# Performance work log

Hardware: AMD Instinct MI355X
Metric: run time of the kernel (lower is better)

Reference implementation:

```python
import jax, jax.numpy as jnp
import numpy as np

DIM = 256
D_STATE = 16
D_CONV = 4
EXPAND = 2
D_INNER = DIM * EXPAND          # 512
DT_RANK = DIM // 16             # 16


def _dwconv(x_bcl, w, b, pad):
    # depthwise 1d conv; x_bcl: (B, C, L), w: (C, 1, K)
    out = jax.lax.conv_general_dilated(
        x_bcl, w, window_strides=(1,), padding=[pad],
        feature_group_count=x_bcl.shape[1],
        dimension_numbers=('NCH', 'OIH', 'NCH'))
    return out + b[None, :, None]


def _forward(x, ln_w, ln_b, W_in, conv_w, conv_b, W_xproj, W_dt, b_dt,
             A_log, D_ssm, W_outp, c1_w, c1_b, c2_w, c2_b, c3_w, c3_b,
             W_out, b_out, W_skip, b_skip):
    Bsz, C = x.shape[:2]
    img_dims = x.shape[2:]
    L = int(np.prod(img_dims))
    xf = x.reshape(Bsz, C, L).transpose(0, 2, 1)          # (B, L, C)
    # LayerNorm over channel dim
    mu = jnp.mean(xf, axis=-1, keepdims=True)
    var = jnp.var(xf, axis=-1, keepdims=True)
    xn = (xf - mu) / jnp.sqrt(var + 1e-5) * ln_w + ln_b   # (B, L, C)

    # ---------------- Mamba block ----------------
    xz = xn @ W_in.T                                      # (B, L, 2*Di)
    xi, z = jnp.split(xz, 2, axis=-1)
    k = conv_w.shape[-1]
    # causal depthwise conv (pad left d_conv-1, truncate to L), then silu
    xc = _dwconv(xi.transpose(0, 2, 1), conv_w, conv_b, (k - 1, 0))
    xc = jax.nn.silu(xc).transpose(0, 2, 1)               # (B, L, Di)
    x_dbl = xc @ W_xproj.T                                # (B, L, dt_rank + 2*N)
    dt = x_dbl[..., :DT_RANK]
    B_s = x_dbl[..., DT_RANK:DT_RANK + D_STATE]           # (B, L, N)
    C_s = x_dbl[..., DT_RANK + D_STATE:]                  # (B, L, N)
    delta = jax.nn.softplus(dt @ W_dt.T + b_dt)           # (B, L, Di)
    A = -jnp.exp(A_log)                                   # (Di, N)
    dA = jnp.exp(delta[..., None] * A)                    # (B, L, Di, N)
    dBu = (delta * xc)[..., None] * B_s[:, :, None, :]    # (B, L, Di, N)

    def step(h, inp):
        dA_t, dBu_t, c_t = inp
        h = dA_t * h + dBu_t                              # (B, Di, N)
        y = jnp.einsum('bdn,bn->bd', h, c_t)
        return h, y

    h0 = jnp.zeros((Bsz, D_INNER, D_STATE), dtype=x.dtype)
    _, ys = jax.lax.scan(
        step, h0,
        (dA.transpose(1, 0, 2, 3), dBu.transpose(1, 0, 2, 3), C_s.transpose(1, 0, 2)))
    y = ys.transpose(1, 0, 2) + D_ssm * xc                # (B, L, Di)
    y = y * jax.nn.silu(z)
    x_ssm = y @ W_outp.T                                  # (B, L, C)

    # ---------------- multi-scale depthwise convs ----------------
    xnT = xn.transpose(0, 2, 1)                           # (B, C, L)

    def msconv(w, b):
        kk = w.shape[-1]
        return jax.nn.silu(_dwconv(xnT, w, b, (kk // 2, kk // 2))).transpose(0, 2, 1)

    combined = x_ssm + msconv(c1_w, c1_b) + msconv(c2_w, c2_b) + msconv(c3_w, c3_b)
    out = combined @ W_out.T + b_out + xn @ W_skip.T + b_skip
    out = out.transpose(0, 2, 1).reshape(x.shape)
    return out + x


def setup_inputs() -> dict:
    key = jax.random.key(0)
    ks = jax.random.split(key, 12)

    def rn(k, shape, s=0.02):
        return jax.random.normal(k, shape, dtype=jnp.float32) * s

    return {
        'x': jax.random.normal(ks[0], (2, DIM, 64, 64), dtype=jnp.float32),
        'ln_w': jnp.ones((DIM,), jnp.float32),
        'ln_b': jnp.zeros((DIM,), jnp.float32),
        'W_in': rn(ks[1], (2 * D_INNER, DIM)),
        'conv_w': rn(ks[2], (D_INNER, 1, D_CONV), 0.1),
        'conv_b': jnp.zeros((D_INNER,), jnp.float32),
        'W_xproj': rn(ks[3], (DT_RANK + 2 * D_STATE, D_INNER)),
        'W_dt': rn(ks[4], (D_INNER, DT_RANK), 0.1),
        'b_dt': jnp.full((D_INNER,), -4.0, jnp.float32),  # softplus(-4) ~ 0.018, stable dt
        'A_log': jnp.log(jnp.broadcast_to(
            jnp.arange(1, D_STATE + 1, dtype=jnp.float32), (D_INNER, D_STATE))),
        'D_ssm': jnp.ones((D_INNER,), jnp.float32),
        'W_outp': rn(ks[5], (DIM, D_INNER)),
        'c1_w': rn(ks[6], (DIM, 1, 3), 0.1),
        'c1_b': jnp.zeros((DIM,), jnp.float32),
        'c2_w': rn(ks[7], (DIM, 1, 5), 0.1),
        'c2_b': jnp.zeros((DIM,), jnp.float32),
        'c3_w': rn(ks[8], (DIM, 1, 7), 0.1),
        'c3_b': jnp.zeros((DIM,), jnp.float32),
        'W_out': rn(ks[9], (DIM, DIM)),
        'b_out': jnp.zeros((DIM,), jnp.float32),
        'W_skip': rn(ks[10], (DIM, DIM)),
        'b_skip': jnp.zeros((DIM,), jnp.float32),
    }


def reference(x, ln_w, ln_b, W_in, conv_w, conv_b, W_xproj, W_dt, b_dt,
              A_log, D_ssm, W_outp, c1_w, c1_b, c2_w, c2_b, c3_w, c3_b,
              W_out, b_out, W_skip, b_skip):
    return _forward(x, ln_w, ln_b, W_in, conv_w, conv_b, W_xproj, W_dt, b_dt,
                    A_log, D_ssm, W_outp, c1_w, c1_b, c2_w, c2_b, c3_w, c3_b,
                    W_out, b_out, W_skip, b_skip)
```

## Files before the change

### kernel.cpp

```cpp
#include <hip/hip_runtime.h>
#include <hip/hip_bf16.h>
#include <math.h>
#include <cstddef>

#define BSZ 2
#define DM 256
#define LSEQ 4096
#define DIN 512
#define DXZ 1024
#define DS 16
#define RANK 16
#define GXP 48
#define LC 32
#define NC 128
#define CSTRIDE (BSZ * DIN * 16)

typedef __attribute__((ext_vector_type(8))) short short8;
typedef __attribute__((ext_vector_type(4))) float f32x4;
struct bf4 { __hip_bfloat16 v[4]; };

__device__ __forceinline__ float silu_f(float x){ return x / (1.f + __expf(-x)); }
__device__ __forceinline__ float softplus_f(float x){ return fmaxf(x, 0.f) + log1pf(__expf(-fabsf(x))); }
__device__ __forceinline__ float b2f(__hip_bfloat16 v){ return __bfloat162float(v); }
__device__ __forceinline__ __hip_bfloat16 f2b(float v){ return __float2bfloat16(v); }

__device__ __forceinline__ void gl_lds16(const void* g, void* s){
    __builtin_amdgcn_global_load_lds((const __attribute__((address_space(1))) void*)g,
                                     (__attribute__((address_space(3))) void*)s, 16, 0, 0);
}

__global__ __launch_bounds__(256) void k_ln(const float* __restrict__ x,
                                            const float* __restrict__ lnw,
                                            const float* __restrict__ lnb,
                                            __hip_bfloat16* __restrict__ xnb){
    __shared__ float tile[DM * 33];
    __shared__ float rsum[8][32], rsq[8][32];
    __shared__ float mu_s[32], rs_s[32];
    int b  = blockIdx.x >> 7;
    int l0 = (blockIdx.x & 127) << 5;
    int tid = threadIdx.x;
    const float* xb = x + (size_t)b * DM * LSEQ;
    int lls = tid & 31, chi = tid >> 5;
    for (int cc = 0; cc < 32; ++cc){
        int c = cc * 8 + chi;
        tile[c * 33 + lls] = xb[(size_t)c * LSEQ + l0 + lls];
    }
    __syncthreads();
    int part = tid >> 5, l = tid & 31;
    float s = 0.f, sq = 0.f;
    for (int i = 0; i < 32; ++i){
        float v = tile[(part * 32 + i) * 33 + l];
        s += v; sq += v * v;
    }
    rsum[part][l] = s; rsq[part][l] = sq;
    __syncthreads();
    if (tid < 32){
        float ts = 0.f, tq = 0.f;
        for (int p = 0; p < 8; ++p){ ts += rsum[p][tid]; tq += rsq[p][tid]; }
        float mu  = ts * (1.f / DM);
        float var = tq * (1.f / DM) - mu * mu;
        mu_s[tid] = mu;
        rs_s[tid] = rsqrtf(var + 1e-5f);
    }
    __syncthreads();
    int c0 = tid & 63, lh = tid >> 6;
    for (int i = 0; i < 8; ++i){
        int ll = lh + 4 * i;
        float mu = mu_s[ll], rs = rs_s[ll];
        __hip_bfloat16* orow = xnb + (size_t)(b * LSEQ + l0 + ll) * 512;
        for (int j = 0; j < 4; ++j){
            int c = c0 + 64 * j;
            orow[c] = f2b((tile[c * 33 + ll] - mu) * rs * lnw[c] + lnb[c]);
        }
    }
}

__global__ __launch_bounds__(256) void k_cvtw(const float* __restrict__ W_in, const float* __restrict__ W_xproj,
                                              const float* __restrict__ W_outp, const float* __restrict__ W_out,
                                              const float* __restrict__ W_skip, const float* __restrict__ b_out,
                                              const float* __restrict__ b_skip,
                                              __hip_bfloat16* __restrict__ Winb, __hip_bfloat16* __restrict__ Wxpb,
                                              __hip_bfloat16* __restrict__ Wopb, __hip_bfloat16* __restrict__ Wcb,
                                              float* __restrict__ bc){
    int i0 = blockIdx.x * 256 + threadIdx.x;
    const int T = 256 * 256;
    for (int j = i0; j < 1024 * 256; j += T) Winb[j] = f2b(W_in[j]);
    for (int j = i0; j < 64 * 512; j += T){
        int r = j >> 9;
        Wxpb[j] = f2b(r < GXP ? W_xproj[r * 512 + (j & 511)] : 0.f);
    }
    for (int j = i0; j < 256 * 512; j += T) Wopb[j] = f2b(W_outp[j]);
    for (int j = i0; j < 256 * 512; j += T){
        int n = j >> 9, k = j & 511;
        Wcb[j] = f2b(k < 256 ? W_out[n * 256 + k] : W_skip[n * 256 + (k - 256)]);
    }
    if (i0 < 256) bc[i0] = b_out[i0] + b_skip[i0];
}

template<int EPI, int BM = 128, int BN = 64>
__global__ __launch_bounds__(256) void k_mgemm(const __hip_bfloat16* __restrict__ A, int lda,
                                               const __hip_bfloat16* __restrict__ W,
                                               const float* __restrict__ bias,
                                               void* __restrict__ Cv, int ldc,
                                               int N, int K,
                                               const float* __restrict__ xres = nullptr){
    constexpr int SA  = BM / 8;
    constexpr int SAW = SA / 4;
    constexpr int SB  = BN / 8;
    constexpr int SBW = SB / 4;
    constexpr int WROWS = BM / 2;
    constexpr int WCOLS = BN / 2;
    constexpr int MI = WROWS / 16;
    constexpr int NI = WCOLS / 16;
    __shared__ __align__(16) __hip_bfloat16 As[BM * 64];
    __shared__ __align__(16) __hip_bfloat16 Ws[BN * 64];
    __shared__ float tileT[(EPI & 16) ? 64 * 65 : 1];
    const int tid = threadIdx.x;
    const int wave = tid >> 6, lane = tid & 63;
    const int brow = blockIdx.x * BM, bcol = blockIdx.y * BN;
    const int wm = wave >> 1, wn = wave & 1;

    const int a_row = lane >> 3;
    const int a_chk = lane & 7;
    const int a_scol = ((a_chk ^ a_row) * 8);

    const int lrow = lane & 15;
    const int kc = lane >> 4;
    const int r7 = lrow & 7;

    f32x4 acc[MI][NI] = {};

    for (int k0 = 0; k0 < K; k0 += 64){
#pragma unroll
        for (int j = 0; j < SAW; ++j){
            int seg = wave * SAW + j;
            const __hip_bfloat16* src = A + (size_t)(brow + seg * 8 + a_row) * lda + k0 + a_scol;
            gl_lds16(src, &As[seg * 512]);
        }
#pragma unroll
        for (int j = 0; j < SBW; ++j){
            int seg = wave * SBW + j;
            const __hip_bfloat16* src = W + (size_t)(bcol + seg * 8 + a_row) * K + k0 + a_scol;
            gl_lds16(src, &Ws[seg * 512]);
        }
        __syncthreads();
#pragma unroll
        for (int kk = 0; kk < 2; ++kk){
            int kchunk = kk * 4 + kc;
            short8 af[MI], bfr[NI];
#pragma unroll
            for (int mi = 0; mi < MI; ++mi){
                int row = wm * WROWS + mi * 16 + lrow;
                af[mi] = *(const short8*)&As[row * 64 + ((kchunk ^ r7) * 8)];
            }
#pragma unroll
            for (int ni = 0; ni < NI; ++ni){
                int row = wn * WCOLS + ni * 16 + lrow;
                bfr[ni] = *(const short8*)&Ws[row * 64 + ((kchunk ^ r7) * 8)];
            }
#pragma unroll
            for (int mi = 0; mi < MI; ++mi)
#pragma unroll
                for (int ni = 0; ni < NI; ++ni)
                    acc[mi][ni] = __builtin_amdgcn_mfma_f32_16x16x32_bf16(af[mi], bfr[ni], acc[mi][ni], 0, 0, 0);
        }
        __syncthreads();
    }

    if (EPI & 16){
#pragma unroll
        for (int ni = 0; ni < NI; ++ni){
            int nl = wn * WCOLS + ni * 16 + lrow;
#pragma unroll
            for (int mi = 0; mi < MI; ++mi){
                int ml = wm * WROWS + mi * 16 + kc * 4;
#pragma unroll
                for (int r = 0; r < 4; ++r)
                    tileT[nl * 65 + ml + r] = acc[mi][ni][r];
            }
        }
        __syncthreads();
        int b = brow >> 12, l0 = brow & 4095;
        int lr = tid & 63, nr = tid >> 6;
        float* out = (float*)Cv;
#pragma unroll
        for (int rr = 0; rr < 16; ++rr){
            int n = rr * 4 + nr;
            size_t o = (size_t)(b * DM + bcol + n) * LSEQ + l0 + lr;
            out[o] = tileT[n * 65 + lr] + bias[bcol + n] + xres[o];
        }
        return;
    }

#pragma unroll
    for (int ni = 0; ni < NI; ++ni){
        int n = bcol + wn * WCOLS + ni * 16 + lrow;
        if (n >= N) continue;
        float bv = (EPI & 1) ? bias[n] : 0.f;
#pragma unroll
        for (int mi = 0; mi < MI; ++mi){
            int m0 = brow + wm * WROWS + mi * 16 + kc * 4;
#pragma unroll
            for (int r = 0; r < 4; ++r){
                float v = acc[mi][ni][r] + bv;
                if (EPI & 8) ((__hip_bfloat16*)Cv)[(size_t)(m0 + r) * ldc + n] = f2b(v);
                else         ((float*)Cv)[(size_t)(m0 + r) * ldc + n] = v;
            }
        }
    }
}

__global__ __launch_bounds__(256) void k_dtgemm(const float* __restrict__ A, int lda,
                                                const float* __restrict__ Wt,
                                                const float* __restrict__ bias,
                                                __hip_bfloat16* __restrict__ C, int ldc){
    __shared__ float As[16][68];
    __shared__ float Ws[16][68];
    int bm = blockIdx.x * 64, bn = blockIdx.y * 64;
    int tid = threadIdx.x;
    int a_m = tid >> 2, a_k = (tid & 3) * 4;
    int tx = tid & 15, ty = tid >> 4;
    float acc[4][4] = {};
    {
        float4 av = *(const float4*)(A + (size_t)(bm + a_m) * lda + a_k);
        As[a_k + 0][a_m] = av.x; As[a_k + 1][a_m] = av.y;
        As[a_k + 2][a_m] = av.z; As[a_k + 3][a_m] = av.w;
        float4 wv = *(const float4*)(Wt + (size_t)(bn + a_m) * 16 + a_k);
        Ws[a_k + 0][a_m] = wv.x; Ws[a_k + 1][a_m] = wv.y;
        Ws[a_k + 2][a_m] = wv.z; Ws[a_k + 3][a_m] = wv.w;
        __syncthreads();
#pragma unroll
        for (int k = 0; k < 16; ++k){
            float4 a4 = *(const float4*)&As[k][ty * 4];
            float4 b4 = *(const float4*)&Ws[k][tx * 4];
            acc[0][0] += a4.x * b4.x; acc[0][1] += a4.x * b4.y; acc[0][2] += a4.x * b4.z; acc[0][3] += a4.x * b4.w;
            acc[1][0] += a4.y * b4.x; acc[1][1] += a4.y * b4.y; acc[1][2] += a4.y * b4.z; acc[1][3] += a4.y * b4.w;
            acc[2][0] += a4.z * b4.x; acc[2][1] += a4.z * b4.y; acc[2][2] += a4.z * b4.z; acc[2][3] += a4.z * b4.w;
            acc[3][0] += a4.w * b4.x; acc[3][1] += a4.w * b4.y; acc[3][2] += a4.w * b4.z; acc[3][3] += a4.w * b4.w;
        }
    }
    int n = bn + tx * 4;
    float4 bb = *(const float4*)(bias + n);
#pragma unroll
    for (int i = 0; i < 4; ++i){
        int m = bm + ty * 4 + i;
        __hip_bfloat16* cp = C + (size_t)m * ldc + n;
        cp[0] = f2b(softplus_f(acc[i][0] + bb.x));
        cp[1] = f2b(softplus_f(acc[i][1] + bb.y));
        cp[2] = f2b(softplus_f(acc[i][2] + bb.z));
        cp[3] = f2b(softplus_f(acc[i][3] + bb.w));
    }
}

__global__ __launch_bounds__(256) void k_conv(const __hip_bfloat16* __restrict__ xz,
                                              const float* __restrict__ cw,
                                              const float* __restrict__ cb,
                                              __hip_bfloat16* __restrict__ xc){
    int idx = blockIdx.x * 256 + threadIdx.x;
    int d4 = (idx & 127) * 4;
    int bl = idx >> 7;
    int l  = bl & (LSEQ - 1);
    const __hip_bfloat16* base = xz + (size_t)bl * DXZ + d4;
    float4 bias = *(const float4*)(cb + d4);
    float acc[4] = {bias.x, bias.y, bias.z, bias.w};
    float4 w0 = *(const float4*)(cw + (d4 + 0) * 4);
    float4 w1 = *(const float4*)(cw + (d4 + 1) * 4);
    float4 w2 = *(const float4*)(cw + (d4 + 2) * 4);
    float4 w3 = *(const float4*)(cw + (d4 + 3) * 4);
    const float* wj[4] = {(const float*)&w0, (const float*)&w1, (const float*)&w2, (const float*)&w3};
#pragma unroll
    for (int t = 0; t < 4; ++t){
        int ls = l - (3 - t);
        if (ls >= 0){
            bf4 v = *(const bf4*)(base - (size_t)(3 - t) * DXZ);
#pragma unroll
            for (int j = 0; j < 4; ++j) acc[j] += wj[j][t] * b2f(v.v[j]);
        }
    }
    bf4 o;
#pragma unroll
    for (int j = 0; j < 4; ++j) o.v[j] = f2b(silu_f(acc[j]));
    *(bf4*)(xc + (size_t)bl * DIN + d4) = o;
}

__global__ __launch_bounds__(512) void k_scan1(const __hip_bfloat16* __restrict__ delta,
                                               const __hip_bfloat16* __restrict__ xc,
                                               const float* __restrict__ xdbl,
                                               const float* __restrict__ A_log,
                                               float* __restrict__ Acar,
                                               float* __restrict__ Bcar){
    int bx = blockIdx.x;
    int dh = bx & 1;
    int c  = (bx >> 1) & (NC - 1);
    int b  = bx >> 8;
    int tid = threadIdx.x;
    int dloc = tid >> 1, nh = tid & 1;
    int d = dh * 256 + dloc;
    int n0 = nh * 8;
    __shared__ float Bs[LC][DS];
    {
        int t = tid >> 4, n = tid & 15;
        Bs[t][n] = xdbl[(size_t)(b * LSEQ + c * LC + t) * GXP + RANK + n];
    }
    __syncthreads();
    float Av[8];
    float a1 = -__expf(A_log[d * 16]);
    bool fast = true;
#pragma unroll
    for (int j = 0; j < 8; ++j){
        Av[j] = -__expf(A_log[d * 16 + n0 + j]);
        fast = fast && (fabsf(Av[j] - (float)(n0 + j + 1) * a1) <= 1e-4f * fabsf(Av[j]) + 1e-7f);
    }
    float ap[8], ac[8];
#pragma unroll
    for (int j = 0; j < 8; ++j){ ap[j] = 1.f; ac[j] = 0.f; }
    const __hip_bfloat16* dp = delta + (size_t)(b * LSEQ + c * LC) * DIN + d;
    const __hip_bfloat16* xp = xc    + (size_t)(b * LSEQ + c * LC) * DIN + d;
    if (fast){
        for (int t = 0; t < LC; ++t){
            float de = b2f(dp[(size_t)t * DIN]);
            float u  = de * b2f(xp[(size_t)t * DIN]);
            float p  = __expf(de * a1);
            float p2 = p * p, p4 = p2 * p2, p8 = p4 * p4;
            float da = nh ? p8 * p : p;
#pragma unroll
            for (int j = 0; j < 8; ++j){
                ap[j] *= da;
                ac[j] = da * ac[j] + u * Bs[t][n0 + j];
                da *= p;
            }
        }
    } else {
        for (int t = 0; t < LC; ++t){
            float de = b2f(dp[(size_t)t * DIN]);
            float u  = de * b2f(xp[(size_t)t * DIN]);
#pragma unroll
            for (int j = 0; j < 8; ++j){
                float da = __expf(de * Av[j]);
                ap[j] *= da;
                ac[j] = da * ac[j] + u * Bs[t][n0 + j];
            }
        }
    }
    size_t o = (size_t)c * CSTRIDE + (size_t)(b * DIN + d) * 16 + n0;
    *(float4*)(Acar + o)     = make_float4(ap[0], ap[1], ap[2], ap[3]);
    *(float4*)(Acar + o + 4) = make_float4(ap[4], ap[5], ap[6], ap[7]);
    *(float4*)(Bcar + o)     = make_float4(ac[0], ac[1], ac[2], ac[3]);
    *(float4*)(Bcar + o + 4) = make_float4(ac[4], ac[5], ac[6], ac[7]);
}

__global__ __launch_bounds__(256) void k_scan2(const float* __restrict__ Acar,
                                               const float* __restrict__ Bcar,
                                               float* __restrict__ hinit){
    __shared__ float a_s[NC][33];
    __shared__ float b_s[NC][33];
    __shared__ float h_s[NC][33];
    const int tid = threadIdx.x;
    const int idx0 = blockIdx.x * 32;
    const int s_ld = tid & 31, cr = tid >> 5;
#pragma unroll
    for (int r = 0; r < 16; ++r){
        int c = r * 8 + cr;
        size_t g = (size_t)c * CSTRIDE + idx0 + s_ld;
        a_s[c][s_ld] = Acar[g];
        b_s[c][s_ld] = Bcar[g];
    }
    __syncthreads();
    const int lane = tid & 63, w = tid >> 6;
#pragma unroll
    for (int i = 0; i < 8; ++i){
        int s = w * 8 + i;
        float a0 = a_s[2 * lane][s],     b0 = b_s[2 * lane][s];
        float a1 = a_s[2 * lane + 1][s], b1 = b_s[2 * lane + 1][s];
        float av = a0 * a1, bv = a1 * b0 + b1;
#pragma unroll
        for (int d2 = 1; d2 < 64; d2 <<= 1){
            float ao = __shfl_up(av, d2);
            float bo = __shfl_up(bv, d2);
            if (lane >= d2){ bv = av * bo + bv; av = ao * av; }
        }
        float ax = __shfl_up(av, 1), bx = __shfl_up(bv, 1);
        if (lane == 0){ ax = 1.f; bx = 0.f; }
        h_s[2 * lane][s]     = bx;
        h_s[2 * lane + 1][s] = a0 * bx + b0;
    }
    __syncthreads();
#pragma unroll
    for (int r = 0; r < 16; ++r){
        int c = r * 8 + cr;
        hinit[(size_t)c * CSTRIDE + idx0 + s_ld] = h_s[c][s_ld];
    }
}

__global__ __launch_bounds__(512) void k_scan3(const __hip_bfloat16* __restrict__ delta,
                                               const __hip_bfloat16* __restrict__ xc,
                                               const __hip_bfloat16* __restrict__ xz,
                                               const float* __restrict__ xdbl,
                                               const float* __restrict__ A_log,
                                               const float* __restrict__ D_ssm,
                                               const float* __restrict__ hinit,
                                               __hip_bfloat16* __restrict__ y){
    int bx = blockIdx.x;
    int dh = bx & 1;
    int c  = (bx >> 1) & (NC - 1);
    int b  = bx >> 8;
    int tid = threadIdx.x;
    int dloc = tid >> 1, nh = tid & 1;
    int d = dh * 256 + dloc;
    int n0 = nh * 8;
    __shared__ float Bs[LC][DS], Cs[LC][DS];
    {
        int t = tid >> 4, n = tid & 15;
        size_t r = (size_t)(b * LSEQ + c * LC + t) * GXP;
        Bs[t][n] = xdbl[r + RANK + n];
        Cs[t][n] = xdbl[r + RANK + DS + n];
    }
    __syncthreads();
    float Av[8];
    float a1 = -__expf(A_log[d * 16]);
    bool fast = true;
#pragma unroll
    for (int j = 0; j < 8; ++j){
        Av[j] = -__expf(A_log[d * 16 + n0 + j]);
        fast = fast && (fabsf(Av[j] - (float)(n0 + j + 1) * a1) <= 1e-4f * fabsf(Av[j]) + 1e-7f);
    }
    float h[8];
    size_t ho = (size_t)c * CSTRIDE + (size_t)(b * DIN + d) * 16 + n0;
    {
        float4 h0 = *(const float4*)(hinit + ho);
        float4 h1 = *(const float4*)(hinit + ho + 4);
        h[0] = h0.x; h[1] = h0.y; h[2] = h0.z; h[3] = h0.w;
        h[4] = h1.x; h[5] = h1.y; h[6] = h1.z; h[7] = h1.w;
    }
    float Dd = D_ssm[d];
    size_t rb = (size_t)(b * LSEQ + c * LC);
    if (fast){
        for (int t = 0; t < LC; ++t){
            size_t row = rb + t;
            float de  = b2f(delta[row * DIN + d]);
            float xcv = b2f(xc[row * DIN + d]);
            float u = de * xcv;
            float p  = __expf(de * a1);
            float p2 = p * p, p4 = p2 * p2, p8 = p4 * p4;
            float da = nh ? p8 * p : p;
            float yv = 0.f;
#pragma unroll
            for (int j = 0; j < 8; ++j){
                h[j] = da * h[j] + u * Bs[t][n0 + j];
                yv += h[j] * Cs[t][n0 + j];
                da *= p;
            }
            yv += __shfl_xor(yv, 1);
            if (nh == 0){
                float zv = b2f(xz[row * DXZ + DIN + d]);
                y[row * DIN + d] = f2b((yv + Dd * xcv) * silu_f(zv));
            }
        }
    } else {
        for (int t = 0; t < LC; ++t){
            size_t row = rb + t;
            float de  = b2f(delta[row * DIN + d]);
            float xcv = b2f(xc[row * DIN + d]);
            float u = de * xcv;
            float yv = 0.f;
#pragma unroll
            for (int j = 0; j < 8; ++j){
                float da = __expf(de * Av[j]);
                h[j] = da * h[j] + u * Bs[t][n0 + j];
                yv += h[j] * Cs[t][n0 + j];
            }
            yv += __shfl_xor(yv, 1);
            if (nh == 0){
                float zv = b2f(xz[row * DXZ + DIN + d]);
                y[row * DIN + d] = f2b((yv + Dd * xcv) * silu_f(zv));
            }
        }
    }
}

__global__ __launch_bounds__(256) void k_msconv(const __hip_bfloat16* __restrict__ xnb,
                                                const __hip_bfloat16* __restrict__ xssm,
                                                const float* __restrict__ c1w, const float* __restrict__ c1b,
                                                const float* __restrict__ c2w, const float* __restrict__ c2b,
                                                const float* __restrict__ c3w, const float* __restrict__ c3b,
                                                __hip_bfloat16* __restrict__ Acomb){
    int idx = blockIdx.x * 256 + threadIdx.x;
    int cch = idx & (DM - 1);
    int bl  = idx >> 8;
    int l   = bl & (LSEQ - 1);
    int bL  = bl - l;
    float a1 = c1b[cch], a2 = c2b[cch], a3 = c3b[cch];
#pragma unroll
    for (int j = -3; j <= 3; ++j){
        int ll = l + j;
        if ((unsigned)ll < LSEQ){
            float v = b2f(xnb[(size_t)(bL + ll) * 512 + cch]);
            if (j >= -1 && j <= 1) a1 += c1w[cch * 3 + (j + 1)] * v;
            if (j >= -2 && j <= 2) a2 += c2w[cch * 5 + (j + 2)] * v;
            a3 += c3w[cch * 7 + (j + 3)] * v;
        }
    }
    float res = b2f(xssm[(size_t)bl * 256 + cch]) + silu_f(a1) + silu_f(a2) + silu_f(a3);
    Acomb[(size_t)bl * 512 + cch] = f2b(res);
}

extern "C" void kernel_launch(void* const* d_in, const int* in_sizes, int n_in,
                              void* d_out, int out_size, void* d_ws, size_t ws_size,
                              hipStream_t stream){
    const float* x      = (const float*)d_in[0];
    const float* ln_w   = (const float*)d_in[1];
    const float* ln_b   = (const float*)d_in[2];
    const float* W_in   = (const float*)d_in[3];
    const float* conv_w = (const float*)d_in[4];
    const float* conv_b = (const float*)d_in[5];
    const float* W_xproj= (const float*)d_in[6];
    const float* W_dt   = (const float*)d_in[7];
    const float* b_dt   = (const float*)d_in[8];
    const float* A_log  = (const float*)d_in[9];
    const float* D_ssm  = (const float*)d_in[10];
    const float* W_outp = (const float*)d_in[11];
    const float* c1_w   = (const float*)d_in[12];
    const float* c1_b   = (const float*)d_in[13];
    const float* c2_w   = (const float*)d_in[14];
    const float* c2_b   = (const float*)d_in[15];
    const float* c3_w   = (const float*)d_in[16];
    const float* c3_b   = (const float*)d_in[17];
    const float* W_out  = (const float*)d_in[18];
    const float* b_out  = (const float*)d_in[19];
    const float* W_skip = (const float*)d_in[20];
    const float* b_skip = (const float*)d_in[21];
    float* out = (float*)d_out;

    char* base = (char*)d_ws;
    const size_t MB = 1024 * 1024;
    __hip_bfloat16* Acomb = (__hip_bfloat16*)(base);
    __hip_bfloat16* xzb   = (__hip_bfloat16*)(base + 8*MB);
    __hip_bfloat16* xcb   = (__hip_bfloat16*)(base + 24*MB);
    float*          xdbl  = (float*)        (base + 32*MB);
    __hip_bfloat16* deltab= (__hip_bfloat16*)(base + 34*MB);
    float*          Acar  = (float*)        (base + 42*MB);
    float*          Bcar  = (float*)        (base + 50*MB);
    float*          hinit = (float*)        (base + 58*MB);
    __hip_bfloat16* xssmb = (__hip_bfloat16*)(base + 66*MB);
    __hip_bfloat16* Winb  = (__hip_bfloat16*)(base + 70*MB);
    __hip_bfloat16* Wxpb  = (__hip_bfloat16*)(base + 70*MB + 512*1024);
    __hip_bfloat16* Wopb  = (__hip_bfloat16*)(base + 71*MB);
    __hip_bfloat16* Wcb   = (__hip_bfloat16*)(base + 71*MB + 256*1024);
    float*          bc    = (float*)        (base + 71*MB + 512*1024);
    __hip_bfloat16* xnb   = Acomb + 256;
    __hip_bfloat16* ybf   = (__hip_bfloat16*)Bcar;

    const int M = BSZ * LSEQ;

    k_cvtw<<<dim3(256), dim3(256), 0, stream>>>(W_in, W_xproj, W_outp, W_out, W_skip, b_out, b_skip,
                                                Winb, Wxpb, Wopb, Wcb, bc);
    k_ln<<<dim3(256), dim3(256), 0, stream>>>(x, ln_w, ln_b, xnb);
    k_mgemm<8, 128, 128><<<dim3(64, 8), dim3(256), 0, stream>>>(xnb, 512, Winb, nullptr, xzb, DXZ, 1024, 256);
    k_conv<<<dim3(M * DIN / 4 / 256), dim3(256), 0, stream>>>(xzb, conv_w, conv_b, xcb);
    k_mgemm<0, 32, 64><<<dim3(256, 1), dim3(256), 0, stream>>>(xcb, 512, Wxpb, nullptr, xdbl, GXP, GXP, 512);
    k_dtgemm<<<dim3(128, 8), dim3(256), 0, stream>>>(xdbl, GXP, W_dt, b_dt, deltab, DIN);
    k_scan1<<<dim3(BSZ * NC * 2), dim3(512), 0, stream>>>(deltab, xcb, xdbl, A_log, Acar, Bcar);
    k_scan2<<<dim3(512), dim3(256), 0, stream>>>(Acar, Bcar, hinit);
    k_scan3<<<dim3(BSZ * NC * 2), dim3(512), 0, stream>>>(deltab, xcb, xzb, xdbl, A_log, D_ssm, hinit, ybf);
    k_mgemm<8, 64, 64><<<dim3(128, 4), dim3(256), 0, stream>>>(ybf, 512, Wopb, nullptr, xssmb, 256, 256, 512);
    k_msconv<<<dim3(M * DM / 256), dim3(256), 0, stream>>>(xnb, xssmb, c1_w, c1_b, c2_w, c2_b, c3_w, c3_b, Acomb);
    k_mgemm<17, 64, 64><<<dim3(128, 4), dim3(256), 0, stream>>>(Acomb, 512, Wcb, bc, out, DM, 256, 512, x);
}
```

Before: 244.7 us.

## Fuse LN with weight conversion, x_proj with dt GEMM, and msconv into out_proj epilogue

Merges the layernorm and weight-conversion kernels into one launch, fuses the x_proj GEMM with the dt projection plus softplus using MFMA on bf16, and folds the multi-scale depthwise conv and SiLU sum into the out_proj GEMM epilogue. This removes three kernel launches and the intermediate xssm and xdbl round-trips through global memory. The cost is heavier epilogue work and scattered bf16 loads of xnb inside the GEMM, plus extra bf16 rounding of the dt input.

```diff
diff --git a/kernel.cpp b/kernel.cpp
--- a/kernel.cpp
+++ b/kernel.cpp
@@ -29,72 +29,88 @@
                                      (__attribute__((address_space(3))) void*)s, 16, 0, 0);
 }
 
-__global__ __launch_bounds__(256) void k_ln(const float* __restrict__ x,
-                                            const float* __restrict__ lnw,
-                                            const float* __restrict__ lnb,
-                                            __hip_bfloat16* __restrict__ xnb){
+__global__ __launch_bounds__(256) void k_pre(const float* __restrict__ x,
+                                             const float* __restrict__ lnw, const float* __restrict__ lnb,
+                                             const float* __restrict__ W_in, const float* __restrict__ W_xproj,
+                                             const float* __restrict__ W_outp, const float* __restrict__ W_out,
+                                             const float* __restrict__ W_skip, const float* __restrict__ b_out,
+                                             const float* __restrict__ b_skip, const float* __restrict__ W_dt,
+                                             const float* __restrict__ c1w, const float* __restrict__ c1b,
+                                             const float* __restrict__ c2w, const float* __restrict__ c2b,
+                                             const float* __restrict__ c3w, const float* __restrict__ c3b,
+                                             __hip_bfloat16* __restrict__ xnb,
+                                             __hip_bfloat16* __restrict__ Winb, __hip_bfloat16* __restrict__ Wxpb,
+                                             __hip_bfloat16* __restrict__ Wopb, __hip_bfloat16* __restrict__ Wcb,
+                                             __hip_bfloat16* __restrict__ Wdtb, float* __restrict__ bc,
+                                             float* __restrict__ msw){
     __shared__ float tile[DM * 33];
     __shared__ float rsum[8][32], rsq[8][32];
     __shared__ float mu_s[32], rs_s[32];
-    int b  = blockIdx.x >> 7;
-    int l0 = (blockIdx.x & 127) << 5;
     int tid = threadIdx.x;
-    const float* xb = x + (size_t)b * DM * LSEQ;
-    int lls = tid & 31, chi = tid >> 5;
-    for (int cc = 0; cc < 32; ++cc){
-        int c = cc * 8 + chi;
-        tile[c * 33 + lls] = xb[(size_t)c * LSEQ + l0 + lls];
-    }
-    __syncthreads();
-    int part = tid >> 5, l = tid & 31;
-    float s = 0.f, sq = 0.f;
-    for (int i = 0; i < 32; ++i){
-        float v = tile[(part * 32 + i) * 33 + l];
-        s += v; sq += v * v;
-    }
-    rsum[part][l] = s; rsq[part][l] = sq;
-    __syncthreads();
-    if (tid < 32){
-        float ts = 0.f, tq = 0.f;
-        for (int p = 0; p < 8; ++p){ ts += rsum[p][tid]; tq += rsq[p][tid]; }
-        float mu  = ts * (1.f / DM);
-        float var = tq * (1.f / DM) - mu * mu;
-        mu_s[tid] = mu;
-        rs_s[tid] = rsqrtf(var + 1e-5f);
-    }
-    __syncthreads();
-    int c0 = tid & 63, lh = tid >> 6;
-    for (int i = 0; i < 8; ++i){
-        int ll = lh + 4 * i;
-        float mu = mu_s[ll], rs = rs_s[ll];
-        __hip_bfloat16* orow = xnb + (size_t)(b * LSEQ + l0 + ll) * 512;
-        for (int j = 0; j < 4; ++j){
-            int c = c0 + 64 * j;
-            orow[c] = f2b((tile[c * 33 + ll] - mu) * rs * lnw[c] + lnb[c]);
-        }
-    }
-}
-
-__global__ __launch_bounds__(256) void k_cvtw(const float* __restrict__ W_in, const float* __restrict__ W_xproj,
-                                              const float* __restrict__ W_outp, const float* __restrict__ W_out,
-                                              const float* __restrict__ W_skip, const float* __restrict__ b_out,
-                                              const float* __restrict__ b_skip,
-                                              __hip_bfloat16* __restrict__ Winb, __hip_bfloat16* __restrict__ Wxpb,
-                                              __hip_bfloat16* __restrict__ Wopb, __hip_bfloat16* __restrict__ Wcb,
-                                              float* __restrict__ bc){
-    int i0 = blockIdx.x * 256 + threadIdx.x;
-    const int T = 256 * 256;
-    for (int j = i0; j < 1024 * 256; j += T) Winb[j] = f2b(W_in[j]);
-    for (int j = i0; j < 64 * 512; j += T){
-        int r = j >> 9;
-        Wxpb[j] = f2b(r < GXP ? W_xproj[r * 512 + (j & 511)] : 0.f);
-    }
-    for (int j = i0; j < 256 * 512; j += T) Wopb[j] = f2b(W_outp[j]);
-    for (int j = i0; j < 256 * 512; j += T){
-        int n = j >> 9, k = j & 511;
-        Wcb[j] = f2b(k < 256 ? W_out[n * 256 + k] : W_skip[n * 256 + (k - 256)]);
-    }
-    if (i0 < 256) bc[i0] = b_out[i0] + b_skip[i0];
+    if (blockIdx.x < 256){
+        int b  = blockIdx.x >> 7;
+        int l0 = (blockIdx.x & 127) << 5;
+        const float* xb = x + (size_t)b * DM * LSEQ;
+        int lls = tid & 31, chi = tid >> 5;
+        for (int cc = 0; cc < 32; ++cc){
+            int c = cc * 8 + chi;
+            tile[c * 33 + lls] = xb[(size_t)c * LSEQ + l0 + lls];
+        }
+        __syncthreads();
+        int part = tid >> 5, l = tid & 31;
+        float s = 0.f, sq = 0.f;
+        for (int i = 0; i < 32; ++i){
+            float v = tile[(part * 32 + i) * 33 + l];
+            s += v; sq += v * v;
+        }
+        rsum[part][l] = s; rsq[part][l] = sq;
+        __syncthreads();
+        if (tid < 32){
+            float ts = 0.f, tq = 0.f;
+            for (int p = 0; p < 8; ++p){ ts += rsum[p][tid]; tq += rsq[p][tid]; }
+            float mu  = ts * (1.f / DM);
+            float var = tq * (1.f / DM) - mu * mu;
+            mu_s[tid] = mu;
+            rs_s[tid] = rsqrtf(var + 1e-5f);
+        }
+        __syncthreads();
+        int c0 = tid & 63, lh = tid >> 6;
+        for (int i = 0; i < 8; ++i){
+            int ll = lh + 4 * i;
+            float mu = mu_s[ll], rs = rs_s[ll];
+            __hip_bfloat16* orow = xnb + (size_t)(b * LSEQ + l0 + ll) * 512;
+            for (int j = 0; j < 4; ++j){
+                int c = c0 + 64 * j;
+                orow[c] = f2b((tile[c * 33 + ll] - mu) * rs * lnw[c] + lnb[c]);
+            }
+        }
+    } else {
+        int i0 = (blockIdx.x - 256) * 256 + tid;
+        const int T = 256 * 256;
+        for (int j = i0; j < 1024 * 256; j += T) Winb[j] = f2b(W_in[j]);
+        for (int j = i0; j < 64 * 512; j += T){
+            int r = j >> 9;
+            Wxpb[j] = f2b(r < GXP ? W_xproj[r * 512 + (j & 511)] : 0.f);
+        }
+        for (int j = i0; j < 256 * 512; j += T) Wopb[j] = f2b(W_outp[j]);
+        for (int j = i0; j < 256 * 512; j += T){
+            int n = j >> 9, k = j & 511;
+            Wcb[j] = f2b(k < 256 ? W_out[n * 256 + k] : W_skip[n * 256 + (k - 256)]);
+        }
+        for (int j = i0; j < 512 * 32; j += T){
+            int n = j >> 5, k = j & 31;
+            Wdtb[j] = f2b(k < 16 ? W_dt[n * 16 + k] : 0.f);
+        }
+        if (i0 < 256){
+            bc[i0] = b_out[i0] + b_skip[i0];
+            float* m = msw + i0 * 20;
+            m[0] = c1w[i0*3]; m[1] = c1w[i0*3+1]; m[2] = c1w[i0*3+2];
+            for (int j = 0; j < 5; ++j) m[3+j] = c2w[i0*5+j];
+            for (int j = 0; j < 7; ++j) m[8+j] = c3w[i0*7+j];
+            m[15] = c1b[i0]; m[16] = c2b[i0]; m[17] = c3b[i0];
+            m[18] = 0.f; m[19] = 0.f;
+        }
+    }
 }
 
 template<int EPI, int BM = 128, int BN = 64>
@@ -103,7 +119,9 @@
                                                const float* __restrict__ bias,
                                                void* __restrict__ Cv, int ldc,
                                                int N, int K,
-                                               const float* __restrict__ xres = nullptr){
+                                               const float* __restrict__ xres = nullptr,
+                                               const __hip_bfloat16* __restrict__ xnb2 = nullptr,
+                                               const float* __restrict__ msw = nullptr){
     constexpr int SA  = BM / 8;
     constexpr int SAW = SA / 4;
     constexpr int SB  = BN / 8;
@@ -192,6 +210,42 @@
         return;
     }
 
+    if (EPI & 32){
+#pragma unroll
+        for (int ni = 0; ni < NI; ++ni){
+            int n = bcol + wn * WCOLS + ni * 16 + lrow;
+            float4 wv0 = *(const float4*)&msw[n * 20];
+            float4 wv1 = *(const float4*)&msw[n * 20 + 4];
+            float4 wv2 = *(const float4*)&msw[n * 20 + 8];
+            float4 wv3 = *(const float4*)&msw[n * 20 + 12];
+            float4 wv4 = *(const float4*)&msw[n * 20 + 16];
+#pragma unroll
+            for (int mi = 0; mi < MI; ++mi){
+                int m0 = brow + wm * WROWS + mi * 16 + kc * 4;
+                int l  = m0 & (LSEQ - 1);
+                int bL = m0 - l;
+                float v[10];
+#pragma unroll
+                for (int k = 0; k < 10; ++k){
+                    int ll = l - 3 + k;
+                    v[k] = ((unsigned)ll < LSEQ) ? b2f(xnb2[(size_t)(bL + ll) * 512 + n]) : 0.f;
+                }
+#pragma unroll
+                for (int r = 0; r < 4; ++r){
+                    float a1 = wv3.w + wv0.x * v[r+2] + wv0.y * v[r+3] + wv0.z * v[r+4];
+                    float a2 = wv4.x + wv0.w * v[r+1] + wv1.x * v[r+2] + wv1.y * v[r+3]
+                                     + wv1.z * v[r+4] + wv1.w * v[r+5];
+                    float a3 = wv4.y + wv2.x * v[r] + wv2.y * v[r+1] + wv2.z * v[r+2]
+                                     + wv2.w * v[r+3] + wv3.x * v[r+4] + wv3.y * v[r+5]
+                                     + wv3.z * v[r+6];
+                    float res = acc[mi][ni][r] + silu_f(a1) + silu_f(a2) + silu_f(a3);
+                    ((__hip_bfloat16*)Cv)[(size_t)(m0 + r) * ldc + n] = f2b(res);
+                }
+            }
+        }
+        return;
+    }
+
 #pragma unroll
     for (int ni = 0; ni < NI; ++ni){
         int n = bcol + wn * WCOLS + ni * 16 + lrow;
@@ -210,45 +264,83 @@
     }
 }
 
-__global__ __launch_bounds__(256) void k_dtgemm(const float* __restrict__ A, int lda,
-                                                const float* __restrict__ Wt,
-                                                const float* __restrict__ bias,
-                                                __hip_bfloat16* __restrict__ C, int ldc){
-    __shared__ float As[16][68];
-    __shared__ float Ws[16][68];
-    int bm = blockIdx.x * 64, bn = blockIdx.y * 64;
-    int tid = threadIdx.x;
-    int a_m = tid >> 2, a_k = (tid & 3) * 4;
-    int tx = tid & 15, ty = tid >> 4;
-    float acc[4][4] = {};
-    {
-        float4 av = *(const float4*)(A + (size_t)(bm + a_m) * lda + a_k);
-        As[a_k + 0][a_m] = av.x; As[a_k + 1][a_m] = av.y;
-        As[a_k + 2][a_m] = av.z; As[a_k + 3][a_m] = av.w;
-        float4 wv = *(const float4*)(Wt + (size_t)(bn + a_m) * 16 + a_k);
-        Ws[a_k + 0][a_m] = wv.x; Ws[a_k + 1][a_m] = wv.y;
-        Ws[a_k + 2][a_m] = wv.z; Ws[a_k + 3][a_m] = wv.w;
-        __syncthreads();
-#pragma unroll
-        for (int k = 0; k < 16; ++k){
-            float4 a4 = *(const float4*)&As[k][ty * 4];
-            float4 b4 = *(const float4*)&Ws[k][tx * 4];
-            acc[0][0] += a4.x * b4.x; acc[0][1] += a4.x * b4.y; acc[0][2] += a4.x * b4.z; acc[0][3] += a4.x * b4.w;
-            acc[1][0] += a4.y * b4.x; acc[1][1] += a4.y * b4.y; acc[1][2] += a4.y * b4.z; acc[1][3] += a4.y * b4.w;
-            acc[2][0] += a4.z * b4.x; acc[2][1] += a4.z * b4.y; acc[2][2] += a4.z * b4.z; acc[2][3] += a4.z * b4.w;
-            acc[3][0] += a4.w * b4.x; acc[3][1] += a4.w * b4.y; acc[3][2] += a4.w * b4.z; acc[3][3] += a4.w * b4.w;
-        }
-    }
-    int n = bn + tx * 4;
-    float4 bb = *(const float4*)(bias + n);
-#pragma unroll
-    for (int i = 0; i < 4; ++i){
-        int m = bm + ty * 4 + i;
-        __hip_bfloat16* cp = C + (size_t)m * ldc + n;
-        cp[0] = f2b(softplus_f(acc[i][0] + bb.x));
-        cp[1] = f2b(softplus_f(acc[i][1] + bb.y));
-        cp[2] = f2b(softplus_f(acc[i][2] + bb.z));
-        cp[3] = f2b(softplus_f(acc[i][3] + bb.w));
+__global__ __launch_bounds__(256) void k_xpdt(const __hip_bfloat16* __restrict__ A,
+                                              const __hip_bfloat16* __restrict__ Wxp,
+                                              const __hip_bfloat16* __restrict__ Wdt,
+                                              const float* __restrict__ bdt,
+                                              float* __restrict__ xdbl,
+                                              __hip_bfloat16* __restrict__ delta){
+    __shared__ __align__(16) __hip_bfloat16 As[32 * 64];
+    __shared__ __align__(16) __hip_bfloat16 Ws[64 * 64];
+    __shared__ __hip_bfloat16 xdl[32][34];
+    const int tid = threadIdx.x, wave = tid >> 6, lane = tid & 63;
+    const int brow = blockIdx.x * 32;
+    const int wm = wave >> 1, wn = wave & 1;
+    const int a_row = lane >> 3, a_chk = lane & 7, a_scol = ((a_chk ^ a_row) * 8);
+    const int lrow = lane & 15, kc = lane >> 4, r7 = lrow & 7;
+
+    for (int i = tid; i < 32 * 18; i += 256){
+        int rr = i / 18, cc = 16 + i % 18;
+        xdl[rr][cc] = f2b(0.f);
+    }
+
+    f32x4 acc[2] = {};
+    for (int k0 = 0; k0 < 512; k0 += 64){
+        {
+            int seg = wave;
+            gl_lds16(A + (size_t)(brow + seg * 8 + a_row) * 512 + k0 + a_scol, &As[seg * 512]);
+        }
+#pragma unroll
+        for (int j = 0; j < 2; ++j){
+            int seg = wave * 2 + j;
+            gl_lds16(Wxp + (size_t)(seg * 8 + a_row) * 512 + k0 + a_scol, &Ws[seg * 512]);
+        }
+        __syncthreads();
+#pragma unroll
+        for (int kk = 0; kk < 2; ++kk){
+            int kchunk = kk * 4 + kc;
+            short8 af = *(const short8*)&As[(wm * 16 + lrow) * 64 + ((kchunk ^ r7) * 8)];
+#pragma unroll
+            for (int ni = 0; ni < 2; ++ni){
+                short8 bfr = *(const short8*)&Ws[(wn * 32 + ni * 16 + lrow) * 64 + ((kchunk ^ r7) * 8)];
+                acc[ni] = __builtin_amdgcn_mfma_f32_16x16x32_bf16(af, bfr, acc[ni], 0, 0, 0);
+            }
+        }
+        __syncthreads();
+    }
+
+#pragma unroll
+    for (int ni = 0; ni < 2; ++ni){
+        int n = wn * 32 + ni * 16 + lrow;
+        if (n < 48){
+#pragma unroll
+            for (int r = 0; r < 4; ++r){
+                int ml = wm * 16 + kc * 4 + r;
+                float fv = acc[ni][r];
+                xdbl[(size_t)(brow + ml) * 48 + n] = fv;
+                if (n < 16) xdl[ml][n] = f2b(fv);
+            }
+        }
+    }
+    __syncthreads();
+
+#pragma unroll
+    for (int ct8 = 0; ct8 < 8; ++ct8){
+        int ct = wave * 8 + ct8;
+        int n = ct * 16 + lrow;
+        short8 bfr = *(const short8*)&Wdt[(size_t)n * 32 + kc * 8];
+        float bv = bdt[n];
+#pragma unroll
+        for (int rt = 0; rt < 2; ++rt){
+            short8 af = *(const short8*)&xdl[rt * 16 + lrow][kc * 8];
+            f32x4 dacc = {};
+            dacc = __builtin_amdgcn_mfma_f32_16x16x32_bf16(af, bfr, dacc, 0, 0, 0);
+#pragma unroll
+            for (int r = 0; r < 4; ++r){
+                int m = brow + rt * 16 + kc * 4 + r;
+                delta[(size_t)m * 512 + n] = f2b(softplus_f(dacc[r] + bv));
+            }
+        }
     }
 }
 
@@ -476,32 +568,6 @@
             }
         }
     }
-}
-
-__global__ __launch_bounds__(256) void k_msconv(const __hip_bfloat16* __restrict__ xnb,
-                                                const __hip_bfloat16* __restrict__ xssm,
-                                                const float* __restrict__ c1w, const float* __restrict__ c1b,
-                                                const float* __restrict__ c2w, const float* __restrict__ c2b,
-                                                const float* __restrict__ c3w, const float* __restrict__ c3b,
-                                                __hip_bfloat16* __restrict__ Acomb){
-    int idx = blockIdx.x * 256 + threadIdx.x;
-    int cch = idx & (DM - 1);
-    int bl  = idx >> 8;
-    int l   = bl & (LSEQ - 1);
-    int bL  = bl - l;
-    float a1 = c1b[cch], a2 = c2b[cch], a3 = c3b[cch];
-#pragma unroll
-    for (int j = -3; j <= 3; ++j){
-        int ll = l + j;
-        if ((unsigned)ll < LSEQ){
-            float v = b2f(xnb[(size_t)(bL + ll) * 512 + cch]);
-            if (j >= -1 && j <= 1) a1 += c1w[cch * 3 + (j + 1)] * v;
-            if (j >= -2 && j <= 2) a2 += c2w[cch * 5 + (j + 2)] * v;
-            a3 += c3w[cch * 7 + (j + 3)] * v;
-        }
-    }
-    float res = b2f(xssm[(size_t)bl * 256 + cch]) + silu_f(a1) + silu_f(a2) + silu_f(a3);
-    Acomb[(size_t)bl * 512 + cch] = f2b(res);
 }
 
 extern "C" void kernel_launch(void* const* d_in, const int* in_sizes, int n_in,
@@ -533,6 +599,7 @@
 
     char* base = (char*)d_ws;
     const size_t MB = 1024 * 1024;
+    const size_t KB = 1024;
     __hip_bfloat16* Acomb = (__hip_bfloat16*)(base);
     __hip_bfloat16* xzb   = (__hip_bfloat16*)(base + 8*MB);
     __hip_bfloat16* xcb   = (__hip_bfloat16*)(base + 24*MB);
@@ -541,28 +608,28 @@
     float*          Acar  = (float*)        (base + 42*MB);
     float*          Bcar  = (float*)        (base + 50*MB);
     float*          hinit = (float*)        (base + 58*MB);
-    __hip_bfloat16* xssmb = (__hip_bfloat16*)(base + 66*MB);
-    __hip_bfloat16* Winb  = (__hip_bfloat16*)(base + 70*MB);
-    __hip_bfloat16* Wxpb  = (__hip_bfloat16*)(base + 70*MB + 512*1024);
-    __hip_bfloat16* Wopb  = (__hip_bfloat16*)(base + 71*MB);
-    __hip_bfloat16* Wcb   = (__hip_bfloat16*)(base + 71*MB + 256*1024);
-    float*          bc    = (float*)        (base + 71*MB + 512*1024);
+    __hip_bfloat16* Winb  = (__hip_bfloat16*)(base + 66*MB);
+    __hip_bfloat16* Wxpb  = (__hip_bfloat16*)(base + 66*MB + 512*KB);
+    __hip_bfloat16* Wopb  = (__hip_bfloat16*)(base + 66*MB + 576*KB);
+    __hip_bfloat16* Wcb   = (__hip_bfloat16*)(base + 66*MB + 832*KB);
+    __hip_bfloat16* Wdtb  = (__hip_bfloat16*)(base + 66*MB + 1088*KB);
+    float*          bc    = (float*)        (base + 66*MB + 1120*KB);
+    float*          msw   = (float*)        (base + 66*MB + 1124*KB);
     __hip_bfloat16* xnb   = Acomb + 256;
     __hip_bfloat16* ybf   = (__hip_bfloat16*)Bcar;
 
     const int M = BSZ * LSEQ;
 
-    k_cvtw<<<dim3(256), dim3(256), 0, stream>>>(W_in, W_xproj, W_outp, W_out, W_skip, b_out, b_skip,
-                                                Winb, Wxpb, Wopb, Wcb, bc);
-    k_ln<<<dim3(256), dim3(256), 0, stream>>>(x, ln_w, ln_b, xnb);
+    k_pre<<<dim3(512), dim3(256), 0, stream>>>(x, ln_w, ln_b, W_in, W_xproj, W_outp, W_out, W_skip,
+                                               b_out, b_skip, W_dt, c1_w, c1_b, c2_w, c2_b, c3_w, c3_b,
+                                               xnb, Winb, Wxpb, Wopb, Wcb, Wdtb, bc, msw);
     k_mgemm<8, 128, 128><<<dim3(64, 8), dim3(256), 0, stream>>>(xnb, 512, Winb, nullptr, xzb, DXZ, 1024, 256);
     k_conv<<<dim3(M * DIN / 4 / 256), dim3(256), 0, stream>>>(xzb, conv_w, conv_b, xcb);
-    k_mgemm<0, 32, 64><<<dim3(256, 1), dim3(256), 0, stream>>>(xcb, 512, Wxpb, nullptr, xdbl, GXP, GXP, 512);
-    k_dtgemm<<<dim3(128, 8), dim3(256), 0, stream>>>(xdbl, GXP, W_dt, b_dt, deltab, DIN);
+    k_xpdt<<<dim3(256), dim3(256), 0, stream>>>(xcb, Wxpb, Wdtb, b_dt, xdbl, deltab);
     k_scan1<<<dim3(BSZ * NC * 2), dim3(512), 0, stream>>>(deltab, xcb, xdbl, A_log, Acar, Bcar);
     k_scan2<<<dim3(512), dim3(256), 0, stream>>>(Acar, Bcar, hinit);
     k_scan3<<<dim3(BSZ * NC * 2), dim3(512), 0, stream>>>(deltab, xcb, xzb, xdbl, A_log, D_ssm, hinit, ybf);
-    k_mgemm<8, 64, 64><<<dim3(128, 4), dim3(256), 0, stream>>>(ybf, 512, Wopb, nullptr, xssmb, 256, 256, 512);
-    k_msconv<<<dim3(M * DM / 256), dim3(256), 0, stream>>>(xnb, xssmb, c1_w, c1_b, c2_w, c2_b, c3_w, c3_b, Acomb);
+    k_mgemm<32, 64, 64><<<dim3(128, 4), dim3(256), 0, stream>>>(ybf, 512, Wopb, nullptr, Acomb, 512, 256, 512,
+                                                                nullptr, xnb, msw);
     k_mgemm<17, 64, 64><<<dim3(128, 4), dim3(256), 0, stream>>>(Acomb, 512, Wcb, bc, out, DM, 256, 512, x);
 }
```

Result: faster. 232.5 us (-5.0%).
